# Kernel optimization log

Hardware: AMD Instinct MI355X
Metric: run time of the kernel (lower is better)

## Reference

```python
import jax, jax.numpy as jnp
import numpy as np

N_FEATURES = 2048


def setup_inputs() -> dict:
    key = jax.random.key(0)
    kx, kd, kl, ku = jax.random.split(key, 4)
    x = jax.random.normal(kx, (32, 1024, N_FEATURES), dtype=jnp.float32)
    # torch initializes these params to zeros; use small random values so
    # gradients/flow are non-degenerate while keeping M diagonally dominant.
    d = 0.1 * jax.random.normal(kd, (N_FEATURES,), dtype=jnp.float32)
    l = 0.1 * jax.random.normal(kl, (N_FEATURES - 1,), dtype=jnp.float32)
    u = 0.1 * jax.random.normal(ku, (N_FEATURES - 1,), dtype=jnp.float32)
    return {"x": x, "d": d, "l": l, "u": u}


def reference(x, d, l, u):
    # Build tridiagonal matrix M (faithful to the torch dense construction)
    diag = jax.nn.softplus(d) + 2.0          # [n]
    off_l = jnp.tanh(l)                       # [n-1], subdiagonal
    off_u = jnp.tanh(u)                       # [n-1], superdiagonal
    M = jnp.diag(diag) + jnp.diag(off_l, -1) + jnp.diag(off_u, 1)  # [n, n]
    # Solve M @ y_t = x^T for each batch: x [B, S, n] -> x_t [B, n, S]
    x_t = jnp.swapaxes(x, -2, -1)
    y_t = jnp.linalg.solve(M, x_t)            # M broadcasts over batch
    return jnp.swapaxes(y_t, -2, -1)          # [B, S, n]
```

## Files before the change

kernel.cpp:

```cpp
#include <hip/hip_runtime.h>
#include <math.h>

#define NF 2048
#define ROWS (32 * 1024)
#define CELLS (NF / 4)
#define PHASES 8
#define NBLOCKS 4096
#define BLKTHREADS 512

typedef float f32x4 __attribute__((ext_vector_type(4)));

__device__ __forceinline__ float dpp_up1(float v, float oldv) {
  return __int_as_float(__builtin_amdgcn_update_dpp(
      __float_as_int(oldv), __float_as_int(v), 0x138, 0xF, 0xF, false));
}
__device__ __forceinline__ float dpp_dn1(float v, float oldv) {
  return __int_as_float(__builtin_amdgcn_update_dpp(
      __float_as_int(oldv), __float_as_int(v), 0x130, 0xF, 0xF, false));
}
__device__ __forceinline__ float bcast_lane(float v, int lane) {
  return __int_as_float(__builtin_amdgcn_readlane(__float_as_int(v), lane));
}

__global__ __launch_bounds__(256) void precompute_kernel(
    const float* __restrict__ d, const float* __restrict__ l,
    const float* __restrict__ u, float* __restrict__ wsg,
    float* __restrict__ wsc, float* __restrict__ wsib) {
  __shared__ float diag_s[NF], tl_s[NF], tu_s[NF], b_s[NF];
  const int tid = threadIdx.x;

  for (int i = tid; i < NF; i += 256) {
    float dv = d[i];
    float sp = (dv > 20.f) ? dv : log1pf(expf(dv));
    diag_s[i] = sp + 2.f;
    tl_s[i] = (i < NF - 1) ? tanhf(l[i]) : 0.f;
    tu_s[i] = (i < NF - 1) ? tanhf(u[i]) : 0.f;
  }
  __syncthreads();

  if (tid < 64) {
    const int lane = tid;
    float T00 = 1.f, T01 = 0.f, T10 = 0.f, T11 = 1.f;
#pragma unroll 1
    for (int j = 0; j < 32; ++j) {
      int i = lane * 32 + j;
      float a = diag_s[i];
      float b = (i > 0) ? -tl_s[i - 1] * tu_s[i - 1] : 0.f;
      float n00 = a * T00 + b * T10;
      float n01 = a * T01 + b * T11;
      T10 = T00; T11 = T01; T00 = n00; T01 = n01;
      float s = 1.f / (fabsf(T00) + fabsf(T01) + 1e-30f);
      T00 *= s; T01 *= s; T10 *= s; T11 *= s;
    }
    for (int ofs = 1; ofs < 64; ofs <<= 1) {
      float U00 = __shfl_up(T00, ofs, 64);
      float U01 = __shfl_up(T01, ofs, 64);
      float U10 = __shfl_up(T10, ofs, 64);
      float U11 = __shfl_up(T11, ofs, 64);
      if (lane >= ofs) {
        float n00 = T00 * U00 + T01 * U10;
        float n01 = T00 * U01 + T01 * U11;
        float n10 = T10 * U00 + T11 * U10;
        float n11 = T10 * U01 + T11 * U11;
        T00 = n00; T01 = n01; T10 = n10; T11 = n11;
        float s = 1.f / (fabsf(T00) + fabsf(T01) + 1e-30f);
        T00 *= s; T01 *= s; T10 *= s; T11 *= s;
      }
    }
    float p1 = __shfl_up(T00, 1, 64);
    float p2 = __shfl_up(T10, 1, 64);
    float bp = (lane == 0) ? 1.f : p1 / p2;
#pragma unroll 1
    for (int j = 0; j < 32; ++j) {
      int i = lane * 32 + j;
      float km1 = (i > 0) ? tl_s[i - 1] * tu_s[i - 1] : 0.f;
      float bv = diag_s[i] - km1 / bp;
      b_s[i] = bv;
      bp = bv;
    }
  }
  __syncthreads();

  for (int i = tid; i < NF; i += 256) {
    float invb = 1.f / b_s[i];
    wsg[i] = (i > 0) ? -tl_s[i - 1] / b_s[i - 1] : 0.f;
    wsc[i] = (i < NF - 1) ? -tu_s[i] * invb : 0.f;
    wsib[i] = invb;
  }
}

__global__ __launch_bounds__(BLKTHREADS) void solve_kernel(
    const float* __restrict__ x, const float* __restrict__ wsg,
    const float* __restrict__ wsc, const float* __restrict__ wsib,
    float* __restrict__ y) {
  __shared__ float4 g_s[CELLS], c_s[CELLS], ib_s[CELLS];

  const int lane = threadIdx.x & 63;
  const unsigned row = (blockIdx.x * BLKTHREADS + threadIdx.x) >> 6;
  const unsigned o = row * (NF / 4) + lane;
  const float4* xb = (const float4*)x;
  float4* yb = (float4*)y;

  float4 v[PHASES];
#pragma unroll
  for (int t = 0; t < PHASES; ++t) v[t] = xb[o + t * 64];
#pragma unroll
  for (int t = 0; t < PHASES; ++t) {
    asm volatile("" : "+v"(v[t].x), "+v"(v[t].y), "+v"(v[t].z), "+v"(v[t].w));
  }

  for (int t = threadIdx.x; t < CELLS; t += BLKTHREADS) {
    g_s[t] = ((const float4*)wsg)[t];
    c_s[t] = ((const float4*)wsc)[t];
    ib_s[t] = ((const float4*)wsib)[t];
  }
  __syncthreads();

  const float4* gs = &g_s[lane];
  const float4* cs = &c_s[lane];
  const float4* ibs = &ib_s[lane];

  {
    float ct = 0.f;
#pragma unroll
    for (int t = 0; t < PHASES; ++t) {
      float4 g = gs[t * 64];
      float4 dv = v[t];
      dv.y = fmaf(g.y, dv.x, dv.y);
      dv.z = fmaf(g.z, dv.y, dv.z);
      dv.w = fmaf(g.w, dv.z, dv.w);
      float A = g.x * g.y * g.z * g.w;
      float A2 = A * dpp_up1(A, 1.f);
      float B = fmaf(A, dpp_up1(dv.w, 0.f), dv.w);
      B = fmaf(A2, ct, B);
      float vin = dpp_up1(B, ct);
      ct = bcast_lane(B, 63);
      float p = g.x;
      dv.x = fmaf(p, vin, dv.x);
      p *= g.y; dv.y = fmaf(p, vin, dv.y);
      p *= g.z; dv.z = fmaf(p, vin, dv.z);
      p *= g.w; dv.w = fmaf(p, vin, dv.w);
      v[t] = dv;
    }
  }

  {
    float ct = 0.f;
#pragma unroll
    for (int t = PHASES - 1; t >= 0; --t) {
      float4 c = cs[t * 64];
      float4 ib = ibs[t * 64];
      float4 dv = v[t];
      float4 w;
      w.w = ib.w * dv.w;
      w.z = fmaf(c.z, w.w, ib.z * dv.z);
      w.y = fmaf(c.y, w.z, ib.y * dv.y);
      w.x = fmaf(c.x, w.y, ib.x * dv.x);
      float A = c.x * c.y * c.z * c.w;
      float A2 = A * dpp_dn1(A, 1.f);
      float B = fmaf(A, dpp_dn1(w.x, 0.f), w.x);
      B = fmaf(A2, ct, B);
      float vin = dpp_dn1(B, ct);
      ct = bcast_lane(B, 0);
      float p = c.w;
      w.w = fmaf(p, vin, w.w);
      p *= c.z; w.z = fmaf(p, vin, w.z);
      p *= c.y; w.y = fmaf(p, vin, w.y);
      p *= c.x; w.x = fmaf(p, vin, w.x);
      __builtin_nontemporal_store(*(const f32x4*)&w, (f32x4*)&yb[o + t * 64]);
    }
  }
}

extern "C" void kernel_launch(void* const* d_in, const int* in_sizes, int n_in,
                              void* d_out, int out_size, void* d_ws,
                              size_t ws_size, hipStream_t stream) {
  const float* x = (const float*)d_in[0];
  const float* d = (const float*)d_in[1];
  const float* l = (const float*)d_in[2];
  const float* u = (const float*)d_in[3];
  float* out = (float*)d_out;

  float* wsg = (float*)d_ws;
  float* wsc = wsg + NF;
  float* wsib = wsc + NF;

  precompute_kernel<<<1, 256, 0, stream>>>(d, l, u, wsg, wsc, wsib);
  solve_kernel<<<NBLOCKS, BLKTHREADS, 0, stream>>>(x, wsg, wsc, wsib, out);
}
```

Measured before the change: 115.0 us.

## Make solve waves persistent over several rows with double-buffered prefetch

Result: slower. 164.1 us (+42.7%).

```diff
diff --git a/kernel.cpp b/kernel.cpp
--- a/kernel.cpp
+++ b/kernel.cpp
@@ -5,8 +5,10 @@
 #define ROWS (32 * 1024)
 #define CELLS (NF / 4)
 #define PHASES 8
-#define NBLOCKS 4096
-#define BLKTHREADS 512
+#define NBLOCKS 1024
+#define BLKTHREADS 256
+#define RPW 8
+#define NWAVES 4096u
 
 typedef float f32x4 __attribute__((ext_vector_type(4)));
 
@@ -89,6 +91,64 @@
   }
 }
 
+__device__ __forceinline__ void load_row(float4 (&v)[PHASES],
+                                         const float4* __restrict__ xb,
+                                         unsigned o) {
+#pragma unroll
+  for (int t = 0; t < PHASES; ++t) v[t] = xb[o + t * 64];
+}
+
+__device__ __forceinline__ void solve_row(float4 (&v)[PHASES],
+                                          const float4* gs, const float4* cs,
+                                          const float4* ibs,
+                                          float4* __restrict__ yb, unsigned o) {
+  float ct = 0.f;
+#pragma unroll
+  for (int t = 0; t < PHASES; ++t) {
+    float4 g = gs[t * 64];
+    float4 dv = v[t];
+    dv.y = fmaf(g.y, dv.x, dv.y);
+    dv.z = fmaf(g.z, dv.y, dv.z);
+    dv.w = fmaf(g.w, dv.z, dv.w);
+    float A = g.x * g.y * g.z * g.w;
+    float A2 = A * dpp_up1(A, 1.f);
+    float B = fmaf(A, dpp_up1(dv.w, 0.f), dv.w);
+    B = fmaf(A2, ct, B);
+    float vin = dpp_up1(B, ct);
+    ct = bcast_lane(B, 63);
+    float p = g.x;
+    dv.x = fmaf(p, vin, dv.x);
+    p *= g.y; dv.y = fmaf(p, vin, dv.y);
+    p *= g.z; dv.z = fmaf(p, vin, dv.z);
+    p *= g.w; dv.w = fmaf(p, vin, dv.w);
+    v[t] = dv;
+  }
+  ct = 0.f;
+#pragma unroll
+  for (int t = PHASES - 1; t >= 0; --t) {
+    float4 c = cs[t * 64];
+    float4 ib = ibs[t * 64];
+    float4 dv = v[t];
+    float4 w;
+    w.w = ib.w * dv.w;
+    w.z = fmaf(c.z, w.w, ib.z * dv.z);
+    w.y = fmaf(c.y, w.z, ib.y * dv.y);
+    w.x = fmaf(c.x, w.y, ib.x * dv.x);
+    float A = c.x * c.y * c.z * c.w;
+    float A2 = A * dpp_dn1(A, 1.f);
+    float B = fmaf(A, dpp_dn1(w.x, 0.f), w.x);
+    B = fmaf(A2, ct, B);
+    float vin = dpp_dn1(B, ct);
+    ct = bcast_lane(B, 0);
+    float p = c.w;
+    w.w = fmaf(p, vin, w.w);
+    p *= c.z; w.z = fmaf(p, vin, w.z);
+    p *= c.y; w.y = fmaf(p, vin, w.y);
+    p *= c.x; w.x = fmaf(p, vin, w.x);
+    __builtin_nontemporal_store(*(const f32x4*)&w, (f32x4*)&yb[o + t * 64]);
+  }
+}
+
 __global__ __launch_bounds__(BLKTHREADS) void solve_kernel(
     const float* __restrict__ x, const float* __restrict__ wsg,
     const float* __restrict__ wsc, const float* __restrict__ wsib,
@@ -96,18 +156,14 @@
   __shared__ float4 g_s[CELLS], c_s[CELLS], ib_s[CELLS];
 
   const int lane = threadIdx.x & 63;
-  const unsigned row = (blockIdx.x * BLKTHREADS + threadIdx.x) >> 6;
-  const unsigned o = row * (NF / 4) + lane;
+  const unsigned wave = (blockIdx.x * BLKTHREADS + threadIdx.x) >> 6;
+  const unsigned ostep = NWAVES * (NF / 4);
+  unsigned o = wave * (NF / 4) + lane;
   const float4* xb = (const float4*)x;
   float4* yb = (float4*)y;
 
-  float4 v[PHASES];
-#pragma unroll
-  for (int t = 0; t < PHASES; ++t) v[t] = xb[o + t * 64];
-#pragma unroll
-  for (int t = 0; t < PHASES; ++t) {
-    asm volatile("" : "+v"(v[t].x), "+v"(v[t].y), "+v"(v[t].z), "+v"(v[t].w));
-  }
+  float4 va[PHASES], vb[PHASES];
+  load_row(va, xb, o);
 
   for (int t = threadIdx.x; t < CELLS; t += BLKTHREADS) {
     g_s[t] = ((const float4*)wsg)[t];
@@ -120,55 +176,16 @@
   const float4* cs = &c_s[lane];
   const float4* ibs = &ib_s[lane];
 
-  {
-    float ct = 0.f;
-#pragma unroll
-    for (int t = 0; t < PHASES; ++t) {
-      float4 g = gs[t * 64];
-      float4 dv = v[t];
-      dv.y = fmaf(g.y, dv.x, dv.y);
-      dv.z = fmaf(g.z, dv.y, dv.z);
-      dv.w = fmaf(g.w, dv.z, dv.w);
-      float A = g.x * g.y * g.z * g.w;
-      float A2 = A * dpp_up1(A, 1.f);
-      float B = fmaf(A, dpp_up1(dv.w, 0.f), dv.w);
-      B = fmaf(A2, ct, B);
-      float vin = dpp_up1(B, ct);
-      ct = bcast_lane(B, 63);
-      float p = g.x;
-      dv.x = fmaf(p, vin, dv.x);
-      p *= g.y; dv.y = fmaf(p, vin, dv.y);
-      p *= g.z; dv.z = fmaf(p, vin, dv.z);
-      p *= g.w; dv.w = fmaf(p, vin, dv.w);
-      v[t] = dv;
-    }
-  }
-
-  {
-    float ct = 0.f;
-#pragma unroll
-    for (int t = PHASES - 1; t >= 0; --t) {
-      float4 c = cs[t * 64];
-      float4 ib = ibs[t * 64];
-      float4 dv = v[t];
-      float4 w;
-      w.w = ib.w * dv.w;
-      w.z = fmaf(c.z, w.w, ib.z * dv.z);
-      w.y = fmaf(c.y, w.z, ib.y * dv.y);
-      w.x = fmaf(c.x, w.y, ib.x * dv.x);
-      float A = c.x * c.y * c.z * c.w;
-      float A2 = A * dpp_dn1(A, 1.f);
-      float B = fmaf(A, dpp_dn1(w.x, 0.f), w.x);
-      B = fmaf(A2, ct, B);
-      float vin = dpp_dn1(B, ct);
-      ct = bcast_lane(B, 0);
-      float p = c.w;
-      w.w = fmaf(p, vin, w.w);
-      p *= c.z; w.z = fmaf(p, vin, w.z);
-      p *= c.y; w.y = fmaf(p, vin, w.y);
-      p *= c.x; w.x = fmaf(p, vin, w.x);
-      __builtin_nontemporal_store(*(const f32x4*)&w, (f32x4*)&yb[o + t * 64]);
-    }
+#pragma unroll
+  for (int r = 0; r < RPW; ++r) {
+    if (r & 1) {
+      if (r < RPW - 1) load_row(va, xb, o + ostep);
+      solve_row(vb, gs, cs, ibs, yb, o);
+    } else {
+      if (r < RPW - 1) load_row(vb, xb, o + ostep);
+      solve_row(va, gs, cs, ibs, yb, o);
+    }
+    o += ostep;
   }
 }
 
```
